# Kernel optimization log

Measured on AMD Instinct MI355X. Metric: run time of the kernel, lower is better.

The kernel has to match this reference:

```python
import jax, jax.numpy as jnp
import numpy as np

N_NODES = 100000
N_EDGES = 1600000
INP, EMB, OUT = 8, 64, 1
N_LAYERS = 4


def setup_inputs() -> dict:
    key = jax.random.key(0)
    ks = jax.random.split(key, 16)
    s = lambda fan_in: 1.0 / np.sqrt(fan_in)
    inp = {
        "x": jax.random.normal(ks[0], (N_NODES, INP), jnp.float32),
        "edge_index": jax.random.randint(ks[1], (2, N_EDGES), 0, N_NODES, jnp.int32),
        "edge_weight": jax.random.uniform(ks[2], (N_EDGES,), jnp.float32),
        # encoder MLP: Linear(INP,EMB) -> ReLU -> Linear(EMB,EMB)
        "enc_w1": jax.random.uniform(ks[3], (INP, EMB), jnp.float32, -s(INP), s(INP)),
        "enc_b1": jnp.zeros((EMB,), jnp.float32),
        "enc_w2": jax.random.uniform(ks[4], (EMB, EMB), jnp.float32, -s(EMB), s(EMB)),
        "enc_b2": jnp.zeros((EMB,), jnp.float32),
        # stacked GCNConv weights/biases
        "gcn_w": jax.random.uniform(ks[5], (N_LAYERS, EMB, EMB), jnp.float32, -s(EMB), s(EMB)),
        "gcn_b": jnp.zeros((N_LAYERS, EMB), jnp.float32),
        # decoder MLP: Linear(EMB,EMB) -> ReLU -> Linear(EMB,OUT)
        "dec_w1": jax.random.uniform(ks[6], (EMB, EMB), jnp.float32, -s(EMB), s(EMB)),
        "dec_b1": jnp.zeros((EMB,), jnp.float32),
        "dec_w2": jax.random.uniform(ks[7], (EMB, OUT), jnp.float32, -s(EMB), s(EMB)),
        "dec_b2": jnp.zeros((OUT,), jnp.float32),
    }
    return inp


def _gcn_norm(edge_index, edge_weight, n_nodes):
    # PyG gcn_norm with add_self_loops=True, symmetric normalization.
    loop = jnp.arange(n_nodes, dtype=edge_index.dtype)
    src = jnp.concatenate([edge_index[0], loop])
    dst = jnp.concatenate([edge_index[1], loop])
    w = jnp.concatenate([edge_weight, jnp.ones((n_nodes,), edge_weight.dtype)])
    deg = jax.ops.segment_sum(w, dst, num_segments=n_nodes)
    dis = jnp.where(deg > 0, jax.lax.rsqrt(jnp.where(deg > 0, deg, 1.0)), 0.0)
    norm = dis[src] * w * dis[dst]  # [E + N]
    return src, dst, norm


def reference(x, edge_index, edge_weight, enc_w1, enc_b1, enc_w2, enc_b2,
              gcn_w, gcn_b, dec_w1, dec_b1, dec_w2, dec_b2):
    n_nodes = x.shape[0]
    src, dst, norm = _gcn_norm(edge_index, edge_weight, n_nodes)

    # encoder MLP
    h = jax.nn.relu(x @ enc_w1 + enc_b1) @ enc_w2 + enc_b2  # [N, EMB]

    # message passing: GCNConv then ReLU, per layer
    for i in range(gcn_w.shape[0]):
        t = h @ gcn_w[i]                             # linear transform [N, EMB]
        msg = norm[:, None] * t[src]                 # gather + weight [E+N, EMB]
        agg = jax.ops.segment_sum(msg, dst, num_segments=n_nodes)
        h = jax.nn.relu(agg + gcn_b[i])

    # decoder MLP
    out = jax.nn.relu(h @ dec_w1 + dec_b1) @ dec_w2 + dec_b2  # [N, OUT]
    return out
```

## Files before the change

### kernel.cpp

```cpp
#include <hip/hip_runtime.h>


constexpr int NN   = 100000;
constexpr int NE   = 1600000;
constexpr int INPD = 8;
constexpr int EMBD = 64;
constexpr float FPSCALE = 16777216.0f;
constexpr int LNODES = 32;
constexpr int BNODES = 256;
constexpr int NBUCK  = (NN + BNODES - 1) / BNODES;
constexpr int BCAP   = 5120;
constexpr int NBLKA  = 512;
constexpr int CHUNKA = (NE + NBLKA - 1) / NBLKA;

typedef float f32x4 __attribute__((ext_vector_type(4)));

#define WAVE_LDS_FENCE() do { \
    asm volatile("s_waitcnt lgkmcnt(0)" ::: "memory"); \
    __builtin_amdgcn_sched_barrier(0); \
} while (0)

__global__ __launch_bounds__(512) void k_hist(const int* __restrict__ ei,
                                              int* __restrict__ hist) {
    __shared__ int lcnt[NBUCK];
    int tid = threadIdx.x;
    int beg = blockIdx.x * CHUNKA;
    int end = beg + CHUNKA; if (end > NE) end = NE;
    for (int i = tid; i < NBUCK; i += 512) lcnt[i] = 0;
    __syncthreads();
    for (int e = beg + tid; e < end; e += 512)
        atomicAdd(&lcnt[ei[NE + e] >> 8], 1);
    __syncthreads();
    for (int i = tid; i < NBUCK; i += 512) hist[blockIdx.x * NBUCK + i] = lcnt[i];
}

__global__ __launch_bounds__(512) void k_colscan(int* __restrict__ hist,
                                                 int* __restrict__ totals) {
    __shared__ int s[512];
    int j = blockIdx.x;
    int b = threadIdx.x;
    int v = hist[b * NBUCK + j];
    s[b] = v;
    __syncthreads();
    for (int off = 1; off < 512; off <<= 1) {
        int t = (b >= off) ? s[b - off] : 0;
        __syncthreads();
        s[b] += t;
        __syncthreads();
    }
    hist[b * NBUCK + j] = s[b] - v;
    if (b == 511) totals[j] = s[b];
}

__global__ __launch_bounds__(512) void k_bscan(const int* __restrict__ totals,
                                               int* __restrict__ bucket_base,
                                               int* __restrict__ row_ptr) {
    __shared__ int s[512];
    int tid = threadIdx.x;
    int v = (tid < NBUCK) ? totals[tid] : 0;
    s[tid] = v;
    __syncthreads();
    for (int off = 1; off < 512; off <<= 1) {
        int t = (tid >= off) ? s[tid - off] : 0;
        __syncthreads();
        s[tid] += t;
        __syncthreads();
    }
    if (tid < NBUCK) bucket_base[tid + 1] = s[tid];
    if (tid == 0) { bucket_base[0] = 0; row_ptr[NN] = NE; }
}

__global__ __launch_bounds__(512) void k_scatter(const int* __restrict__ ei,
                                                 const float* __restrict__ w,
                                                 const int* __restrict__ hist,
                                                 int2* __restrict__ brec) {
    __shared__ int lbase[NBUCK];
    __shared__ int lcnt[NBUCK];
    int tid = threadIdx.x;
    int beg = blockIdx.x * CHUNKA;
    int end = beg + CHUNKA; if (end > NE) end = NE;
    for (int i = tid; i < NBUCK; i += 512) {
        lbase[i] = hist[blockIdx.x * NBUCK + i];
        lcnt[i] = 0;
    }
    __syncthreads();
    for (int e = beg + tid; e < end; e += 512) {
        int s = ei[e];
        int d = ei[NE + e];
        int b = d >> 8, dl = d & 255;
        int pos = lbase[b] + atomicAdd(&lcnt[b], 1);
        if (pos < BCAP)
            brec[(size_t)b * BCAP + pos] = make_int2(s | (dl << 17), __float_as_int(w[e]));
    }
}

__global__ __launch_bounds__(256) void k_passB(const int2* __restrict__ brec,
                                               const int* __restrict__ totals,
                                               const int* __restrict__ bucket_base,
                                               float* __restrict__ dis,
                                               int* __restrict__ row_ptr,
                                               int2* __restrict__ csr) {
    __shared__ int2 sbuf[BCAP];
    __shared__ unsigned int sdeg[BNODES];
    __shared__ int scnt[BNODES];
    __shared__ int sincl[BNODES];
    __shared__ int scur[BNODES];
    int b = blockIdx.x;
    int tid = threadIdx.x;
    int n = totals[b]; if (n > BCAP) n = BCAP;
    int nodes = NN - b * BNODES; if (nodes > BNODES) nodes = BNODES;
    const int2* rec = brec + (size_t)b * BCAP;

    sdeg[tid] = 0; scnt[tid] = 0;
    __syncthreads();
    for (int i = tid; i < n; i += 256) {
        int2 r = rec[i];
        int dl = (r.x >> 17) & 255;
        unsigned int fx = (unsigned int)(__int_as_float(r.y) * FPSCALE + 0.5f);
        atomicAdd(&sdeg[dl], fx);
        atomicAdd(&scnt[dl], 1);
    }
    __syncthreads();
    sincl[tid] = scnt[tid];
    __syncthreads();
    for (int off = 1; off < 256; off <<= 1) {
        int t = (tid >= off) ? sincl[tid - off] : 0;
        __syncthreads();
        sincl[tid] += t;
        __syncthreads();
    }
    int excl = sincl[tid] - scnt[tid];
    scur[tid] = excl;
    int base = bucket_base[b];
    if (tid < nodes) {
        float deg = 1.0f + (float)sdeg[tid] * (1.0f / FPSCALE);
        dis[b * BNODES + tid] = 1.0f / sqrtf(deg);
        row_ptr[b * BNODES + tid] = base + excl;
    }
    __syncthreads();
    for (int i = tid; i < n; i += 256) {
        int2 r = rec[i];
        int dl = (r.x >> 17) & 255;
        int p = atomicAdd(&scur[dl], 1);
        sbuf[p] = r;
    }
    __syncthreads();
    for (int i = tid; i < n; i += 256) csr[base + i] = sbuf[i];
}

__global__ __launch_bounds__(256) void k_norm(const int* __restrict__ bucket_base,
                                              const float* __restrict__ dis,
                                              int2* __restrict__ csr) {
    int b = blockIdx.x;
    int tid = threadIdx.x;
    int base = bucket_base[b];
    int n = bucket_base[b + 1] - base;
    for (int i = tid; i < n; i += 256) {
        int2 r = csr[base + i];
        int s = r.x & 0x1FFFF;
        int dl = (r.x >> 17) & 255;
        float v = dis[s] * __int_as_float(r.y) * dis[b * BNODES + dl];
        csr[base + i] = make_int2(r.x, __float_as_int(v));
    }
}

__global__ __launch_bounds__(256) void k_encoder(const float* __restrict__ x,
                                                 const float* __restrict__ w1,
                                                 const float* __restrict__ b1,
                                                 const float* __restrict__ w2,
                                                 const float* __restrict__ b2,
                                                 float* __restrict__ h) {
    __shared__ float sW1[INPD * EMBD];
    __shared__ float sW2[EMBD * EMBD];
    __shared__ float sB1[EMBD];
    __shared__ float sB2[EMBD];
    __shared__ float sZ[32][EMBD];
    int tid = threadIdx.x;
    for (int i = tid; i < INPD * EMBD; i += 256) sW1[i] = w1[i];
    for (int i = tid; i < EMBD * EMBD; i += 256) sW2[i] = w2[i];
    if (tid < EMBD) { sB1[tid] = b1[tid]; sB2[tid] = b2[tid]; }
    __syncthreads();
    int base = blockIdx.x * 32;
    #pragma unroll
    for (int it = 0; it < 8; ++it) {
        int item = tid + it * 256;
        int nl = item >> 6, j = item & 63;
        int node = base + nl;
        float acc = sB1[j];
        if (node < NN) {
            const float* xr = x + (size_t)node * INPD;
            #pragma unroll
            for (int k = 0; k < INPD; ++k) acc += xr[k] * sW1[k * EMBD + j];
        }
        sZ[nl][j] = fmaxf(acc, 0.0f);
    }
    __syncthreads();
    #pragma unroll
    for (int it = 0; it < 8; ++it) {
        int item = tid + it * 256;
        int nl = item >> 6, j2 = item & 63;
        int node = base + nl;
        if (node < NN) {
            float acc = sB2[j2];
            for (int j = 0; j < EMBD; ++j) acc += sZ[nl][j] * sW2[j * EMBD + j2];
            h[(size_t)node * EMBD + j2] = acc;
        }
    }
}

__global__ __launch_bounds__(512) void k_layer(const float* __restrict__ hin,
                                               const float* __restrict__ dis,
                                               const int* __restrict__ row_ptr,
                                               const int2* __restrict__ edges,
                                               const float* __restrict__ W,
                                               const float* __restrict__ bias,
                                               float* __restrict__ hout) {
    __shared__ float sW[EMBD * EMBD];
    __shared__ float sB[EMBD];
    __shared__ float sA[LNODES][EMBD];
    int tid = threadIdx.x;
    for (int i = tid; i < EMBD * EMBD; i += 512) sW[i] = W[i];
    if (tid < EMBD) sB[tid] = bias[tid];
    __syncthreads();

    int g = tid >> 4, l = tid & 15;
    int node = blockIdx.x * LNODES + g;
    const f32x4* h4 = (const f32x4*)hin;
    f32x4 a0 = (f32x4)(0.f), a1 = (f32x4)(0.f), a2 = (f32x4)(0.f), a3 = (f32x4)(0.f);
    if (node < NN) {
        float dsn = dis[node];
        float sn = dsn * dsn;
        a0 = sn * h4[(size_t)node * 16 + l];
        int beg = row_ptr[node], end = row_ptr[node + 1];
        int e = beg;
        for (; e + 4 <= end; e += 4) {
            int2 e0 = edges[e], e1 = edges[e + 1], e2 = edges[e + 2], e3 = edges[e + 3];
            f32x4 t0 = h4[(size_t)(e0.x & 0x1FFFF) * 16 + l];
            f32x4 t1 = h4[(size_t)(e1.x & 0x1FFFF) * 16 + l];
            f32x4 t2 = h4[(size_t)(e2.x & 0x1FFFF) * 16 + l];
            f32x4 t3 = h4[(size_t)(e3.x & 0x1FFFF) * 16 + l];
            a0 += __int_as_float(e0.y) * t0;
            a1 += __int_as_float(e1.y) * t1;
            a2 += __int_as_float(e2.y) * t2;
            a3 += __int_as_float(e3.y) * t3;
        }
        for (; e < end; ++e) {
            int2 ev = edges[e];
            f32x4 tv = h4[(size_t)(ev.x & 0x1FFFF) * 16 + l];
            a0 += __int_as_float(ev.y) * tv;
        }
    }
    a0 += a1 + a2 + a3;
    ((f32x4*)&sA[g][0])[l] = a0;
    WAVE_LDS_FENCE();

    int w = tid >> 6, lane = tid & 63;
    int rbase = w * 4;
    int nbase = blockIdx.x * LNODES + rbase;
    #pragma unroll
    for (int r = 0; r < 4; ++r) {
        const f32x4* row = (const f32x4*)&sA[rbase + r][0];
        float o = sB[lane];
        #pragma unroll
        for (int kk = 0; kk < 16; ++kk) {
            f32x4 av = row[kk];
            o += av.x * sW[(kk * 4 + 0) * EMBD + lane];
            o += av.y * sW[(kk * 4 + 1) * EMBD + lane];
            o += av.z * sW[(kk * 4 + 2) * EMBD + lane];
            o += av.w * sW[(kk * 4 + 3) * EMBD + lane];
        }
        int onode = nbase + r;
        if (onode < NN) hout[(size_t)onode * EMBD + lane] = fmaxf(o, 0.0f);
    }
}

__global__ __launch_bounds__(512) void k_layer_dec(const float* __restrict__ hin,
                                                   const float* __restrict__ dis,
                                                   const int* __restrict__ row_ptr,
                                                   const int2* __restrict__ edges,
                                                   const float* __restrict__ W,
                                                   const float* __restrict__ bias,
                                                   const float* __restrict__ w1d,
                                                   const float* __restrict__ b1d,
                                                   const float* __restrict__ w2d,
                                                   const float* __restrict__ b2d,
                                                   float* __restrict__ out) {
    __shared__ float sW[EMBD * EMBD];
    __shared__ float sW1d[EMBD * EMBD];
    __shared__ float sB[EMBD];
    __shared__ float sB1d[EMBD];
    __shared__ float sW2d[EMBD];
    __shared__ float sA[LNODES][EMBD];
    int tid = threadIdx.x;
    for (int i = tid; i < EMBD * EMBD; i += 512) { sW[i] = W[i]; sW1d[i] = w1d[i]; }
    if (tid < EMBD) { sB[tid] = bias[tid]; sB1d[tid] = b1d[tid]; sW2d[tid] = w2d[tid]; }
    __syncthreads();

    int g = tid >> 4, l = tid & 15;
    int node = blockIdx.x * LNODES + g;
    const f32x4* h4 = (const f32x4*)hin;
    f32x4 a0 = (f32x4)(0.f), a1 = (f32x4)(0.f), a2 = (f32x4)(0.f), a3 = (f32x4)(0.f);
    if (node < NN) {
        float dsn = dis[node];
        float sn = dsn * dsn;
        a0 = sn * h4[(size_t)node * 16 + l];
        int beg = row_ptr[node], end = row_ptr[node + 1];
        int e = beg;
        for (; e + 4 <= end; e += 4) {
            int2 e0 = edges[e], e1 = edges[e + 1], e2 = edges[e + 2], e3 = edges[e + 3];
            f32x4 t0 = h4[(size_t)(e0.x & 0x1FFFF) * 16 + l];
            f32x4 t1 = h4[(size_t)(e1.x & 0x1FFFF) * 16 + l];
            f32x4 t2 = h4[(size_t)(e2.x & 0x1FFFF) * 16 + l];
            f32x4 t3 = h4[(size_t)(e3.x & 0x1FFFF) * 16 + l];
            a0 += __int_as_float(e0.y) * t0;
            a1 += __int_as_float(e1.y) * t1;
            a2 += __int_as_float(e2.y) * t2;
            a3 += __int_as_float(e3.y) * t3;
        }
        for (; e < end; ++e) {
            int2 ev = edges[e];
            f32x4 tv = h4[(size_t)(ev.x & 0x1FFFF) * 16 + l];
            a0 += __int_as_float(ev.y) * tv;
        }
    }
    a0 += a1 + a2 + a3;
    ((f32x4*)&sA[g][0])[l] = a0;
    WAVE_LDS_FENCE();

    int w = tid >> 6, lane = tid & 63;
    int rbase = w * 4;

    float hv[4];
    #pragma unroll
    for (int r = 0; r < 4; ++r) {
        const f32x4* row = (const f32x4*)&sA[rbase + r][0];
        float o = sB[lane];
        #pragma unroll
        for (int kk = 0; kk < 16; ++kk) {
            f32x4 av = row[kk];
            o += av.x * sW[(kk * 4 + 0) * EMBD + lane];
            o += av.y * sW[(kk * 4 + 1) * EMBD + lane];
            o += av.z * sW[(kk * 4 + 2) * EMBD + lane];
            o += av.w * sW[(kk * 4 + 3) * EMBD + lane];
        }
        hv[r] = fmaxf(o, 0.0f);
    }
    WAVE_LDS_FENCE();
    #pragma unroll
    for (int r = 0; r < 4; ++r) sA[rbase + r][lane] = hv[r];
    WAVE_LDS_FENCE();

    float zv[4];
    #pragma unroll
    for (int r = 0; r < 4; ++r) {
        const f32x4* row = (const f32x4*)&sA[rbase + r][0];
        float o = sB1d[lane];
        #pragma unroll
        for (int kk = 0; kk < 16; ++kk) {
            f32x4 av = row[kk];
            o += av.x * sW1d[(kk * 4 + 0) * EMBD + lane];
            o += av.y * sW1d[(kk * 4 + 1) * EMBD + lane];
            o += av.z * sW1d[(kk * 4 + 2) * EMBD + lane];
            o += av.w * sW1d[(kk * 4 + 3) * EMBD + lane];
        }
        zv[r] = fmaxf(o, 0.0f);
    }
    WAVE_LDS_FENCE();
    #pragma unroll
    for (int r = 0; r < 4; ++r) sA[rbase + r][lane] = zv[r];
    WAVE_LDS_FENCE();

    float r = 0.0f;
    #pragma unroll
    for (int u = 0; u < 4; ++u) r += sA[g][l * 4 + u] * sW2d[l * 4 + u];
    r += __shfl_xor(r, 1);
    r += __shfl_xor(r, 2);
    r += __shfl_xor(r, 4);
    r += __shfl_xor(r, 8);
    if (l == 0 && node < NN) out[node] = r + b2d[0];
}

extern "C" void kernel_launch(void* const* d_in, const int* in_sizes, int n_in,
                              void* d_out, int out_size, void* d_ws, size_t ws_size,
                              hipStream_t stream) {
    const float* x      = (const float*)d_in[0];
    const int*   ei     = (const int*)  d_in[1];
    const float* ew     = (const float*)d_in[2];
    const float* enc_w1 = (const float*)d_in[3];
    const float* enc_b1 = (const float*)d_in[4];
    const float* enc_w2 = (const float*)d_in[5];
    const float* enc_b2 = (const float*)d_in[6];
    const float* gcn_w  = (const float*)d_in[7];
    const float* gcn_b  = (const float*)d_in[8];
    const float* dec_w1 = (const float*)d_in[9];
    const float* dec_b1 = (const float*)d_in[10];
    const float* dec_w2 = (const float*)d_in[11];
    const float* dec_b2 = (const float*)d_in[12];
    float* out = (float*)d_out;

    char* ws = (char*)d_ws;
    size_t off = 0;
    auto alloc = [&](size_t bytes) -> void* {
        void* p = (void*)(ws + off);
        off += (bytes + 511) & ~(size_t)511;
        return p;
    };
    int*   hist        = (int*)  alloc((size_t)NBLKA * NBUCK * 4);
    int*   totals      = (int*)  alloc(NBUCK * 4);
    int*   bucket_base = (int*)  alloc((NBUCK + 1) * 4);
    int2*  brec        = (int2*) alloc((size_t)NBUCK * BCAP * 8);
    float* dis         = (float*)alloc(NN * 4);
    int*   row_ptr     = (int*)  alloc((NN + 1) * 4);
    int2*  csr         = (int2*) alloc((size_t)NE * 8);
    float* hbuf        = (float*)alloc((size_t)NN * EMBD * 4);
    float* hbuf2       = (float*)alloc((size_t)NN * EMBD * 4);
    (void)ws_size; (void)n_in; (void)in_sizes; (void)out_size;

    int gE32 = (NN + 31) / 32;
    int gL   = (NN + LNODES - 1) / LNODES;

    k_hist<<<NBLKA, 512, 0, stream>>>(ei, hist);
    k_colscan<<<NBUCK, 512, 0, stream>>>(hist, totals);
    k_bscan<<<1, 512, 0, stream>>>(totals, bucket_base, row_ptr);
    k_scatter<<<NBLKA, 512, 0, stream>>>(ei, ew, hist, brec);
    k_passB<<<NBUCK, 256, 0, stream>>>(brec, totals, bucket_base, dis, row_ptr, csr);
    k_norm<<<NBUCK, 256, 0, stream>>>(bucket_base, dis, csr);

    k_encoder<<<gE32, 256, 0, stream>>>(x, enc_w1, enc_b1, enc_w2, enc_b2, hbuf);

    float* cur = hbuf;
    float* nxt = hbuf2;
    for (int layer = 0; layer < 3; ++layer) {
        k_layer<<<gL, 512, 0, stream>>>(cur, dis, row_ptr, csr,
                                        gcn_w + (size_t)layer * EMBD * EMBD,
                                        gcn_b + (size_t)layer * EMBD, nxt);
        float* tmp = cur; cur = nxt; nxt = tmp;
    }
    k_layer_dec<<<gL, 512, 0, stream>>>(cur, dis, row_ptr, csr,
                                        gcn_w + (size_t)3 * EMBD * EMBD,
                                        gcn_b + (size_t)3 * EMBD,
                                        dec_w1, dec_b1, dec_w2, dec_b2, out);
}
```

Baseline: 437.8 us.

## Split GCN layers into feature-sliced gather and dense kernels with slab layout

Stores node features in eight feature slabs of 8 floats (32 bytes per node per slab). Each layer is split into a gather kernel, where one thread aggregates one destination node over one slab so the working set per slab is small and cache-friendly, and a separate dense kernel that applies the weight matrix, bias and ReLU. The aim is to raise L2 hit rate on the random source-row gathers. The cost is an extra aggregate buffer round-trip through memory, twice the kernel launches, and eight passes over the edge list per layer.

```diff
diff --git a/kernel.cpp b/kernel.cpp
--- a/kernel.cpp
+++ b/kernel.cpp
@@ -6,14 +6,17 @@
 constexpr int INPD = 8;
 constexpr int EMBD = 64;
 constexpr float FPSCALE = 16777216.0f;
-constexpr int LNODES = 32;
 constexpr int BNODES = 256;
 constexpr int NBUCK  = (NN + BNODES - 1) / BNODES;
 constexpr int BCAP   = 5120;
 constexpr int NBLKA  = 512;
 constexpr int CHUNKA = (NE + NBLKA - 1) / NBLKA;
+constexpr int NSLAB  = 8;
+constexpr int GCH    = 256;
+constexpr int NGCH   = (NN + GCH - 1) / GCH;
 
 typedef float f32x4 __attribute__((ext_vector_type(4)));
+typedef int   i32x2 __attribute__((ext_vector_type(2)));
 
 #define WAVE_LDS_FENCE() do { \
     asm volatile("s_waitcnt lgkmcnt(0)" ::: "memory"); \
@@ -164,12 +167,12 @@
     }
 }
 
-__global__ __launch_bounds__(256) void k_encoder(const float* __restrict__ x,
-                                                 const float* __restrict__ w1,
-                                                 const float* __restrict__ b1,
-                                                 const float* __restrict__ w2,
-                                                 const float* __restrict__ b2,
-                                                 float* __restrict__ h) {
+__global__ __launch_bounds__(256) void k_encoderT(const float* __restrict__ x,
+                                                  const float* __restrict__ w1,
+                                                  const float* __restrict__ b1,
+                                                  const float* __restrict__ w2,
+                                                  const float* __restrict__ b2,
+                                                  float* __restrict__ hT) {
     __shared__ float sW1[INPD * EMBD];
     __shared__ float sW2[EMBD * EMBD];
     __shared__ float sB1[EMBD];
@@ -203,60 +206,71 @@
         if (node < NN) {
             float acc = sB2[j2];
             for (int j = 0; j < EMBD; ++j) acc += sZ[nl][j] * sW2[j * EMBD + j2];
-            h[(size_t)node * EMBD + j2] = acc;
+            hT[((size_t)(j2 >> 3) * NN + node) * 8 + (j2 & 7)] = acc;
         }
     }
 }
 
-__global__ __launch_bounds__(512) void k_layer(const float* __restrict__ hin,
-                                               const float* __restrict__ dis,
-                                               const int* __restrict__ row_ptr,
-                                               const int2* __restrict__ edges,
+__global__ __launch_bounds__(256) void k_gather(const f32x4* __restrict__ hT,
+                                                const float* __restrict__ dis,
+                                                const int* __restrict__ row_ptr,
+                                                const i32x2* __restrict__ edges,
+                                                f32x4* __restrict__ aggT) {
+    int f = blockIdx.x & 7;
+    int dst = (blockIdx.x >> 3) * GCH + threadIdx.x;
+    if (dst >= NN) return;
+    const f32x4* hs = hT + (size_t)f * NN * 2;
+    float dsn = dis[dst];
+    float sn = dsn * dsn;
+    f32x4 a0 = sn * hs[(size_t)dst * 2];
+    f32x4 a1 = sn * hs[(size_t)dst * 2 + 1];
+    int e   = __builtin_nontemporal_load(row_ptr + dst);
+    int end = __builtin_nontemporal_load(row_ptr + dst + 1);
+    for (; e + 2 <= end; e += 2) {
+        i32x2 e0 = __builtin_nontemporal_load(edges + e);
+        i32x2 e1 = __builtin_nontemporal_load(edges + e + 1);
+        int s0 = e0.x & 0x1FFFF, s1 = e1.x & 0x1FFFF;
+        f32x4 t00 = hs[(size_t)s0 * 2], t01 = hs[(size_t)s0 * 2 + 1];
+        f32x4 t10 = hs[(size_t)s1 * 2], t11 = hs[(size_t)s1 * 2 + 1];
+        float v0 = __int_as_float(e0.y), v1 = __int_as_float(e1.y);
+        a0 += v0 * t00; a1 += v0 * t01;
+        a0 += v1 * t10; a1 += v1 * t11;
+    }
+    if (e < end) {
+        i32x2 ev = __builtin_nontemporal_load(edges + e);
+        int s = ev.x & 0x1FFFF;
+        float v = __int_as_float(ev.y);
+        a0 += v * hs[(size_t)s * 2];
+        a1 += v * hs[(size_t)s * 2 + 1];
+    }
+    f32x4* as = aggT + (size_t)f * NN * 2;
+    as[(size_t)dst * 2]     = a0;
+    as[(size_t)dst * 2 + 1] = a1;
+}
+
+__global__ __launch_bounds__(512) void k_dense(const f32x4* __restrict__ aggT,
                                                const float* __restrict__ W,
                                                const float* __restrict__ bias,
-                                               float* __restrict__ hout) {
+                                               float* __restrict__ hTo) {
     __shared__ float sW[EMBD * EMBD];
     __shared__ float sB[EMBD];
-    __shared__ float sA[LNODES][EMBD];
+    __shared__ float sA[32][EMBD];
     int tid = threadIdx.x;
     for (int i = tid; i < EMBD * EMBD; i += 512) sW[i] = W[i];
     if (tid < EMBD) sB[tid] = bias[tid];
-    __syncthreads();
-
-    int g = tid >> 4, l = tid & 15;
-    int node = blockIdx.x * LNODES + g;
-    const f32x4* h4 = (const f32x4*)hin;
-    f32x4 a0 = (f32x4)(0.f), a1 = (f32x4)(0.f), a2 = (f32x4)(0.f), a3 = (f32x4)(0.f);
-    if (node < NN) {
-        float dsn = dis[node];
-        float sn = dsn * dsn;
-        a0 = sn * h4[(size_t)node * 16 + l];
-        int beg = row_ptr[node], end = row_ptr[node + 1];
-        int e = beg;
-        for (; e + 4 <= end; e += 4) {
-            int2 e0 = edges[e], e1 = edges[e + 1], e2 = edges[e + 2], e3 = edges[e + 3];
-            f32x4 t0 = h4[(size_t)(e0.x & 0x1FFFF) * 16 + l];
-            f32x4 t1 = h4[(size_t)(e1.x & 0x1FFFF) * 16 + l];
-            f32x4 t2 = h4[(size_t)(e2.x & 0x1FFFF) * 16 + l];
-            f32x4 t3 = h4[(size_t)(e3.x & 0x1FFFF) * 16 + l];
-            a0 += __int_as_float(e0.y) * t0;
-            a1 += __int_as_float(e1.y) * t1;
-            a2 += __int_as_float(e2.y) * t2;
-            a3 += __int_as_float(e3.y) * t3;
-        }
-        for (; e < end; ++e) {
-            int2 ev = edges[e];
-            f32x4 tv = h4[(size_t)(ev.x & 0x1FFFF) * 16 + l];
-            a0 += __int_as_float(ev.y) * tv;
-        }
-    }
-    a0 += a1 + a2 + a3;
-    ((f32x4*)&sA[g][0])[l] = a0;
-    WAVE_LDS_FENCE();
+    int nbase = blockIdx.x * 32;
+    {
+        int f = tid >> 6, within = tid & 63;
+        int nl = within >> 1, half = within & 1;
+        int node = nbase + nl;
+        f32x4 v = (f32x4)(0.f);
+        if (node < NN) v = aggT[((size_t)f * NN + node) * 2 + half];
+        *((f32x4*)&sA[nl][f * 8 + half * 4]) = v;
+    }
+    __syncthreads();
 
     int w = tid >> 6, lane = tid & 63;
     int rbase = w * 4;
-    int nbase = blockIdx.x * LNODES + rbase;
     #pragma unroll
     for (int r = 0; r < 4; ++r) {
         const f32x4* row = (const f32x4*)&sA[rbase + r][0];
@@ -269,15 +283,13 @@
             o += av.z * sW[(kk * 4 + 2) * EMBD + lane];
             o += av.w * sW[(kk * 4 + 3) * EMBD + lane];
         }
-        int onode = nbase + r;
-        if (onode < NN) hout[(size_t)onode * EMBD + lane] = fmaxf(o, 0.0f);
-    }
-}
-
-__global__ __launch_bounds__(512) void k_layer_dec(const float* __restrict__ hin,
-                                                   const float* __restrict__ dis,
-                                                   const int* __restrict__ row_ptr,
-                                                   const int2* __restrict__ edges,
+        int onode = nbase + rbase + r;
+        if (onode < NN)
+            hTo[((size_t)(lane >> 3) * NN + onode) * 8 + (lane & 7)] = fmaxf(o, 0.0f);
+    }
+}
+
+__global__ __launch_bounds__(512) void k_dense_dec(const f32x4* __restrict__ aggT,
                                                    const float* __restrict__ W,
                                                    const float* __restrict__ bias,
                                                    const float* __restrict__ w1d,
@@ -286,50 +298,26 @@
                                                    const float* __restrict__ b2d,
                                                    float* __restrict__ out) {
     __shared__ float sW[EMBD * EMBD];
-    __shared__ float sW1d[EMBD * EMBD];
     __shared__ float sB[EMBD];
     __shared__ float sB1d[EMBD];
     __shared__ float sW2d[EMBD];
-    __shared__ float sA[LNODES][EMBD];
-    int tid = threadIdx.x;
-    for (int i = tid; i < EMBD * EMBD; i += 512) { sW[i] = W[i]; sW1d[i] = w1d[i]; }
+    __shared__ float sA[32][EMBD];
+    int tid = threadIdx.x;
+    for (int i = tid; i < EMBD * EMBD; i += 512) sW[i] = W[i];
     if (tid < EMBD) { sB[tid] = bias[tid]; sB1d[tid] = b1d[tid]; sW2d[tid] = w2d[tid]; }
-    __syncthreads();
-
-    int g = tid >> 4, l = tid & 15;
-    int node = blockIdx.x * LNODES + g;
-    const f32x4* h4 = (const f32x4*)hin;
-    f32x4 a0 = (f32x4)(0.f), a1 = (f32x4)(0.f), a2 = (f32x4)(0.f), a3 = (f32x4)(0.f);
-    if (node < NN) {
-        float dsn = dis[node];
-        float sn = dsn * dsn;
-        a0 = sn * h4[(size_t)node * 16 + l];
-        int beg = row_ptr[node], end = row_ptr[node + 1];
-        int e = beg;
-        for (; e + 4 <= end; e += 4) {
-            int2 e0 = edges[e], e1 = edges[e + 1], e2 = edges[e + 2], e3 = edges[e + 3];
-            f32x4 t0 = h4[(size_t)(e0.x & 0x1FFFF) * 16 + l];
-            f32x4 t1 = h4[(size_t)(e1.x & 0x1FFFF) * 16 + l];
-            f32x4 t2 = h4[(size_t)(e2.x & 0x1FFFF) * 16 + l];
-            f32x4 t3 = h4[(size_t)(e3.x & 0x1FFFF) * 16 + l];
-            a0 += __int_as_float(e0.y) * t0;
-            a1 += __int_as_float(e1.y) * t1;
-            a2 += __int_as_float(e2.y) * t2;
-            a3 += __int_as_float(e3.y) * t3;
-        }
-        for (; e < end; ++e) {
-            int2 ev = edges[e];
-            f32x4 tv = h4[(size_t)(ev.x & 0x1FFFF) * 16 + l];
-            a0 += __int_as_float(ev.y) * tv;
-        }
-    }
-    a0 += a1 + a2 + a3;
-    ((f32x4*)&sA[g][0])[l] = a0;
-    WAVE_LDS_FENCE();
+    int nbase = blockIdx.x * 32;
+    {
+        int f = tid >> 6, within = tid & 63;
+        int nl = within >> 1, half = within & 1;
+        int node = nbase + nl;
+        f32x4 v = (f32x4)(0.f);
+        if (node < NN) v = aggT[((size_t)f * NN + node) * 2 + half];
+        *((f32x4*)&sA[nl][f * 8 + half * 4]) = v;
+    }
+    __syncthreads();
 
     int w = tid >> 6, lane = tid & 63;
     int rbase = w * 4;
-
     float hv[4];
     #pragma unroll
     for (int r = 0; r < 4; ++r) {
@@ -345,10 +333,11 @@
         }
         hv[r] = fmaxf(o, 0.0f);
     }
-    WAVE_LDS_FENCE();
+    __syncthreads();
+    for (int i = tid; i < EMBD * EMBD; i += 512) sW[i] = w1d[i];
     #pragma unroll
     for (int r = 0; r < 4; ++r) sA[rbase + r][lane] = hv[r];
-    WAVE_LDS_FENCE();
+    __syncthreads();
 
     float zv[4];
     #pragma unroll
@@ -358,10 +347,10 @@
         #pragma unroll
         for (int kk = 0; kk < 16; ++kk) {
             f32x4 av = row[kk];
-            o += av.x * sW1d[(kk * 4 + 0) * EMBD + lane];
-            o += av.y * sW1d[(kk * 4 + 1) * EMBD + lane];
-            o += av.z * sW1d[(kk * 4 + 2) * EMBD + lane];
-            o += av.w * sW1d[(kk * 4 + 3) * EMBD + lane];
+            o += av.x * sW[(kk * 4 + 0) * EMBD + lane];
+            o += av.y * sW[(kk * 4 + 1) * EMBD + lane];
+            o += av.z * sW[(kk * 4 + 2) * EMBD + lane];
+            o += av.w * sW[(kk * 4 + 3) * EMBD + lane];
         }
         zv[r] = fmaxf(o, 0.0f);
     }
@@ -370,6 +359,8 @@
     for (int r = 0; r < 4; ++r) sA[rbase + r][lane] = zv[r];
     WAVE_LDS_FENCE();
 
+    int g = tid >> 4, l = tid & 15;
+    int node = nbase + g;
     float r = 0.0f;
     #pragma unroll
     for (int u = 0; u < 4; ++u) r += sA[g][l * 4 + u] * sW2d[l * 4 + u];
@@ -412,12 +403,13 @@
     float* dis         = (float*)alloc(NN * 4);
     int*   row_ptr     = (int*)  alloc((NN + 1) * 4);
     int2*  csr         = (int2*) alloc((size_t)NE * 8);
-    float* hbuf        = (float*)alloc((size_t)NN * EMBD * 4);
-    float* hbuf2       = (float*)alloc((size_t)NN * EMBD * 4);
+    f32x4* hT_a        = (f32x4*)alloc((size_t)NSLAB * NN * 32);
+    f32x4* hT_b        = (f32x4*)alloc((size_t)NSLAB * NN * 32);
+    f32x4* aggT        = (f32x4*)alloc((size_t)NSLAB * NN * 32);
     (void)ws_size; (void)n_in; (void)in_sizes; (void)out_size;
 
     int gE32 = (NN + 31) / 32;
-    int gL   = (NN + LNODES - 1) / LNODES;
+    int gD   = (NN + 31) / 32;
 
     k_hist<<<NBLKA, 512, 0, stream>>>(ei, hist);
     k_colscan<<<NBUCK, 512, 0, stream>>>(hist, totals);
@@ -426,17 +418,19 @@
     k_passB<<<NBUCK, 256, 0, stream>>>(brec, totals, bucket_base, dis, row_ptr, csr);
     k_norm<<<NBUCK, 256, 0, stream>>>(bucket_base, dis, csr);
 
-    k_encoder<<<gE32, 256, 0, stream>>>(x, enc_w1, enc_b1, enc_w2, enc_b2, hbuf);
-
-    float* cur = hbuf;
-    float* nxt = hbuf2;
+    k_encoderT<<<gE32, 256, 0, stream>>>(x, enc_w1, enc_b1, enc_w2, enc_b2, (float*)hT_a);
+
+    f32x4* cur = hT_a;
+    f32x4* nxt = hT_b;
     for (int layer = 0; layer < 3; ++layer) {
-        k_layer<<<gL, 512, 0, stream>>>(cur, dis, row_ptr, csr,
+        k_gather<<<NGCH * NSLAB, GCH, 0, stream>>>(cur, dis, row_ptr, (const i32x2*)csr, aggT);
+        k_dense<<<gD, 512, 0, stream>>>(aggT,
                                         gcn_w + (size_t)layer * EMBD * EMBD,
-                                        gcn_b + (size_t)layer * EMBD, nxt);
-        float* tmp = cur; cur = nxt; nxt = tmp;
-    }
-    k_layer_dec<<<gL, 512, 0, stream>>>(cur, dis, row_ptr, csr,
+                                        gcn_b + (size_t)layer * EMBD, (float*)nxt);
+        f32x4* tmp = cur; cur = nxt; nxt = tmp;
+    }
+    k_gather<<<NGCH * NSLAB, GCH, 0, stream>>>(cur, dis, row_ptr, (const i32x2*)csr, aggT);
+    k_dense_dec<<<gD, 512, 0, stream>>>(aggT,
                                         gcn_w + (size_t)3 * EMBD * EMBD,
                                         gcn_b + (size_t)3 * EMBD,
                                         dec_w1, dec_b1, dec_w2, dec_b2, out);
```

Result: slower. 1.064 ms (+142.9%).
